# Performance work log

Hardware: AMD Instinct MI355X
Metric: run time of the kernel (lower is better)

The kernel has to match this reference:

```python
import jax, jax.numpy as jnp
import numpy as np
from jax import lax

B, CIN, IMG, K = 128, 3, 112, 7
C = 1024      # hidden_channels * channel_dilation
HID = 512     # hidden_channels
HW = (IMG // K) ** 2  # 256 patches
EPS = 1e-5


def _prelu(x, a):
    return jnp.where(x > 0, x, a * x)


def _bn(x, g, b):
    # BatchNorm2d with track_running_stats=False: always uses batch stats
    m = x.mean(axis=(0, 2, 3), keepdims=True)
    v = x.var(axis=(0, 2, 3), keepdims=True)
    return (x - m) * lax.rsqrt(v + EPS) * g[None, :, None, None] + b[None, :, None, None]


def setup_inputs() -> dict:
    key = jax.random.key(0)
    ks = jax.random.split(key, 16)
    d = {
        'x':  jax.random.normal(ks[0], (B, CIN, IMG, IMG), jnp.float32),
        'w0': jax.random.normal(ks[1], (C, CIN, K, K), jnp.float32) * 0.05,
        'b0': jax.random.normal(ks[2], (C,), jnp.float32) * 0.01,
        'a0': jnp.full((1,), 0.25, jnp.float32),
    }
    for i in range(1, 4):
        kw, kb = jax.random.split(jax.random.fold_in(key, i))
        d[f'w{i}'] = jax.random.normal(kw, (C, C), jnp.float32) * 0.02
        d[f'b{i}'] = jax.random.normal(kb, (C,), jnp.float32) * 0.01
        d[f'g{i}'] = jnp.ones((C,), jnp.float32)
        d[f'bt{i}'] = jnp.zeros((C,), jnp.float32)
        d[f'p{i}'] = jnp.full((1,), 0.25, jnp.float32)
    d['pos'] = jax.random.normal(ks[3], (1, HW, C), jnp.float32)
    d['am'] = jnp.full((1,), 0.25, jnp.float32)
    d['wm'] = jax.random.normal(ks[4], (HID, C), jnp.float32) * 0.03
    d['bm'] = jax.random.normal(ks[5], (HID,), jnp.float32) * 0.01
    pkeys = jax.random.split(ks[6], B)
    d['perm'] = jax.vmap(lambda k: jax.random.permutation(k, HW))(pkeys).astype(jnp.int32)
    return d


def reference(x, w0, b0, a0,
              w1, b1, g1, bt1, p1,
              w2, b2, g2, bt2, p2,
              w3, b3, g3, bt3, p3,
              pos, am, wm, bm, perm):
    # patch-embed conv: stride = kernel_size -> [B, C, 16, 16]
    h = lax.conv_general_dilated(x, w0, (K, K), 'VALID',
                                 dimension_numbers=('NCHW', 'OIHW', 'NCHW'))
    h = _prelu(h + b0[None, :, None, None], a0)
    for w, b, g, bt, p in ((w1, b1, g1, bt1, p1),
                           (w2, b2, g2, bt2, p2),
                           (w3, b3, g3, bt3, p3)):
        h = jnp.einsum('bchw,dc->bdhw', h, w) + b[None, :, None, None]  # 1x1 conv
        h = _prelu(_bn(h, g, bt), p)
    Bn, Cn, Hn, Wn = h.shape
    enc = h.reshape(Bn, Cn, Hn * Wn).transpose(0, 2, 1)  # [B, HW, C]
    enc = enc + pos                                      # private: add pos embedding
    enc = _prelu(enc, am) @ wm.T + bm                    # mixer -> [B, HW, HID]
    # private: per-sample token permutation (single batched gather)
    return jnp.take_along_axis(enc, perm[:, :, None], axis=1)
```

## Files before the change

kernel.cpp:

```cpp
#include <hip/hip_runtime.h>
#include <hip/hip_bf16.h>
#include <stdint.h>


typedef __attribute__((ext_vector_type(8))) short bf16x8;
typedef __attribute__((ext_vector_type(4))) float f32x4;

__device__ __forceinline__ float bf2f(uint32_t u) {
  union { uint32_t i; float f; } v; v.i = u << 16; return v.f;
}
__device__ __forceinline__ ushort f2bf(float f) {
  union { float f; uint32_t i; } v; v.f = f;
  uint32_t i = v.i;
  return (ushort)((i + 0x7FFFu + ((i >> 16) & 1u)) >> 16);
}

template<int EPI, int XB, int K, int DOUT>
__global__ void __launch_bounds__(512, 2)
gemm_kernel(const ushort* __restrict__ A, const ushort* __restrict__ Bw,
            const float* __restrict__ bias, const float* __restrict__ alpha,
            void* __restrict__ outp, float* __restrict__ part,
            const int* __restrict__ inv)
{
  __shared__ __align__(16) ushort At[2][256 * 64];
  __shared__ __align__(16) ushort Bt[3][256 * 64];
  const int tid  = threadIdx.x;
  const int lane = tid & 63;
  const int wid  = tid >> 6;
  const int wm   = wid >> 2;
  const int wn   = wid & 3;

  const int s = blockIdx.x;
  const int j = s >> 3;
  const int x = j & ((1 << XB) - 1);
  const int y = ((j >> XB) << 3) | (s & 7);
  const int t0 = y << 8;
  const int d0 = x << 8;

  f32x4 acc[8][4] = {};

  const int swz = (((lane >> 4) ^ (lane & 7)) << 4);
  const char* LA0 = (const char*)&At[0][0] + ((((wm << 7) + (lane & 15))) << 7) + swz;
  const char* LA1 = (const char*)&At[0][0] + ((((wm << 7) + (lane & 15))) << 7) + (swz ^ 64);
  const char* LB0 = (const char*)&Bt[0][0] + ((((wn << 6) + (lane & 15))) << 7) + swz;
  const char* LB1 = (const char*)&Bt[0][0] + ((((wn << 6) + (lane & 15))) << 7) + (swz ^ 64);

  const int lrow8 = lane >> 3;
  const int csrc  = (lane & 7) ^ lrow8;
  const ushort* gAw = A  + (size_t)(t0 + (wid << 4) + lrow8) * K + (csrc << 3);
  const ushort* gBw = Bw + (size_t)(d0 + (wid << 4) + lrow8) * K + (csrc << 3);
  char* stA = (char*)&At[0][0] + (wid << 11);
  char* stB = (char*)&Bt[0][0] + (wid << 11);

#define STAGE_A(T, BUF, H) do {                                                          \
    __builtin_amdgcn_global_load_lds(                                                    \
      (const __attribute__((address_space(1))) uint32_t*)(gAw + (size_t)((H)*128)*K + ((size_t)(T) << 6)),     \
      (__attribute__((address_space(3))) uint32_t*)(stA + (BUF)*32768 + (H)*16384), 16, 0, 0);                  \
    __builtin_amdgcn_global_load_lds(                                                    \
      (const __attribute__((address_space(1))) uint32_t*)(gAw + (size_t)((H)*128+8)*K + ((size_t)(T) << 6)),   \
      (__attribute__((address_space(3))) uint32_t*)(stA + (BUF)*32768 + (H)*16384 + 1024), 16, 0, 0);           \
  } while (0)
#define STAGE_B(T, BOFF, H) do {                                                         \
    __builtin_amdgcn_global_load_lds(                                                    \
      (const __attribute__((address_space(1))) uint32_t*)(gBw + (size_t)((H)*128)*K + ((size_t)(T) << 6)),     \
      (__attribute__((address_space(3))) uint32_t*)(stB + (BOFF) + (H)*16384), 16, 0, 0);                       \
    __builtin_amdgcn_global_load_lds(                                                    \
      (const __attribute__((address_space(1))) uint32_t*)(gBw + (size_t)((H)*128+8)*K + ((size_t)(T) << 6)),   \
      (__attribute__((address_space(3))) uint32_t*)(stB + (BOFF) + (H)*16384 + 1024), 16, 0, 0);                \
  } while (0)

#define RD_A(dst, BASE, CUR, MH) do {                                                    \
    dst[0] = *(const bf16x8*)((BASE) + (CUR)*32768 + (MH)*8192 + 0);                     \
    dst[1] = *(const bf16x8*)((BASE) + (CUR)*32768 + (MH)*8192 + 2048);                  \
    dst[2] = *(const bf16x8*)((BASE) + (CUR)*32768 + (MH)*8192 + 4096);                  \
    dst[3] = *(const bf16x8*)((BASE) + (CUR)*32768 + (MH)*8192 + 6144);                  \
  } while (0)
#define RD_B(dst, BASE, BOFF) do {                                                       \
    dst[0] = *(const bf16x8*)((BASE) + (BOFF) + 0);                                      \
    dst[1] = *(const bf16x8*)((BASE) + (BOFF) + 2048);                                   \
    dst[2] = *(const bf16x8*)((BASE) + (BOFF) + 4096);                                   \
    dst[3] = *(const bf16x8*)((BASE) + (BOFF) + 6144);                                   \
  } while (0)
#define MFMA16(AF, BF, MH) do {                                                          \
    __builtin_amdgcn_s_setprio(1);                                                       \
    _Pragma("unroll")                                                                    \
    for (int m_ = 0; m_ < 4; ++m_)                                                       \
      _Pragma("unroll")                                                                  \
      for (int n_ = 0; n_ < 4; ++n_)                                                     \
        acc[((MH) << 2) + m_][n_] = __builtin_amdgcn_mfma_f32_16x16x32_bf16(             \
            AF[m_], BF[n_], acc[((MH) << 2) + m_][n_], 0, 0, 0);                         \
    __builtin_amdgcn_s_setprio(0);                                                       \
  } while (0)

#define TILE_BODY(T, CUR, HN1, HN2) do {                                                 \
    if (HN1) { asm volatile("s_waitcnt vmcnt(4)" ::: "memory"); }                        \
    else     { asm volatile("s_waitcnt vmcnt(0)" ::: "memory"); }                        \
    __builtin_amdgcn_s_barrier();                                                        \
    RD_A(aX, LA0, CUR, 0);                                                               \
    RD_B(b0f, LB0, bR);                                                                  \
    if (HN1) { STAGE_A((T) + 1, (CUR) ^ 1, 0); STAGE_A((T) + 1, (CUR) ^ 1, 1); }         \
    if (HN2) { STAGE_B((T) + 2, bS, 0); STAGE_B((T) + 2, bS, 1); }                       \
    MFMA16(aX, b0f, 0);                                                                  \
    RD_A(aY, LA0, CUR, 1);                                                               \
    MFMA16(aY, b0f, 1);                                                                  \
    RD_A(aX, LA1, CUR, 0);                                                               \
    RD_B(b1f, LB1, bR);                                                                  \
    MFMA16(aX, b1f, 0);                                                                  \
    RD_A(aY, LA1, CUR, 1);                                                               \
    MFMA16(aY, b1f, 1);                                                                  \
    { int tmp_ = bR; bR = bN; bN = bS; bS = tmp_; }                                      \
  } while (0)

  constexpr int NT = K >> 6;

  STAGE_A(0, 0, 0); STAGE_A(0, 0, 1);
  STAGE_B(0, 0, 0); STAGE_B(0, 0, 1);
  STAGE_B(1, 32768, 0); STAGE_B(1, 32768, 1);

  int bR = 0, bN = 32768, bS = 65536;
  bf16x8 aX[4], aY[4], b0f[4], b1f[4];

  if constexpr ((NT & 1) == 0) {
#pragma unroll 1
    for (int tp = 0; tp < NT; tp += 2) {
      const bool m1 = (tp + 2 < NT);
      TILE_BODY(tp,     0, true, m1);
      TILE_BODY(tp + 1, 1, m1, m1);
    }
  } else {
#pragma unroll 1
    for (int t = 0; t < NT; ++t) {
      const int cur = t & 1;
      TILE_BODY(t, cur, (t + 1 < NT), (t + 2 < NT));
    }
  }

  float bs[4];
#pragma unroll
  for (int n = 0; n < 4; ++n) bs[n] = bias[d0 + (wn << 6) + (n << 4) + (lane & 15)];
  float a0v = (EPI == 0) ? alpha[0] : 0.0f;
  float sA[4] = {0.f, 0.f, 0.f, 0.f}, s2A[4] = {0.f, 0.f, 0.f, 0.f};

#pragma unroll
  for (int m = 0; m < 8; ++m) {
#pragma unroll
    for (int r = 0; r < 4; ++r) {
      int row = t0 + (wm << 7) + (m << 4) + ((lane >> 4) << 2) + r;
      int orow = (EPI == 2) ? ((row & ~255) | inv[row]) : row;
#pragma unroll
      for (int n = 0; n < 4; ++n) {
        int d = d0 + (wn << 6) + (n << 4) + (lane & 15);
        float v = acc[m][n][r] + bs[n];
        if (EPI == 0) v = v > 0.f ? v : a0v * v;
        if (EPI == 1) { sA[n] += v; s2A[n] += v * v; }
        if (EPI == 2) ((float*)outp)[(size_t)orow * DOUT + d] = v;
        else          ((ushort*)outp)[(size_t)row * DOUT + d] = f2bf(v);
      }
    }
  }

  if (EPI == 1) {
    float2* sm = (float2*)&At[0][0];
    int slot = (wm << 2) | (lane >> 4);
    __syncthreads();
#pragma unroll
    for (int n = 0; n < 4; ++n) {
      int c = (wn << 6) + (n << 4) + (lane & 15);
      sm[slot * 256 + c] = make_float2(sA[n], s2A[n]);
    }
    __syncthreads();
    if (tid < 256) {
      float ss = 0.f, ss2 = 0.f;
      for (int q = 0; q < 8; ++q) {
        float2 v = sm[q * 256 + tid];
        ss += v.x; ss2 += v.y;
      }
      part[(size_t)y * 2048 + d0 + tid]        = ss;
      part[(size_t)y * 2048 + 1024 + d0 + tid] = ss2;
    }
  }
#undef STAGE_A
#undef STAGE_B
#undef RD_A
#undef RD_B
#undef MFMA16
#undef TILE_BODY
}

__global__ void bnfold_kernel(const float* __restrict__ part, const float* __restrict__ g,
                              const float* __restrict__ bt, float* __restrict__ scsh) {
  int d = (blockIdx.x << 8) + threadIdx.x;
  float s = 0.f, s2 = 0.f;
  for (int j = 0; j < 128; ++j) { s += part[j * 2048 + d]; s2 += part[j * 2048 + 1024 + d]; }
  float mean = s * (1.f / 32768.f);
  float var  = s2 * (1.f / 32768.f) - mean * mean;
  float sc = g[d] * rsqrtf(var + 1e-5f);
  scsh[d] = sc;
  scsh[1024 + d] = bt[d] - mean * sc;
}

template<bool MIX>
__global__ void bnact_kernel(ushort* __restrict__ Y, const float* __restrict__ scsh,
                             const float* __restrict__ p, const float* __restrict__ pos,
                             const float* __restrict__ am) {
  float pp = p[0];
  float aa = MIX ? am[0] : 0.f;
#pragma unroll 1
  for (int it = 0; it < 8; ++it) {
    size_t vi = ((size_t)it << 19) + ((size_t)blockIdx.x << 8) + threadIdx.x;
    size_t i = vi << 3;
    int d = (int)(i & 1023);
    float pv[8];
    if (MIX) {
      int prow = (int)((i >> 10) & 255);
      const float4* pb = (const float4*)(pos + ((size_t)prow << 10) + d);
      float4 pA = pb[0], pB = pb[1];
      pv[0]=pA.x; pv[1]=pA.y; pv[2]=pA.z; pv[3]=pA.w;
      pv[4]=pB.x; pv[5]=pB.y; pv[6]=pB.z; pv[7]=pB.w;
    }
    uint4 raw = *(const uint4*)(Y + i);
    uint32_t w[4] = {raw.x, raw.y, raw.z, raw.w};
    uint32_t o[4];
#pragma unroll
    for (int q = 0; q < 4; ++q) {
      int dd = d + q * 2;
      float v0 = bf2f(w[q] & 0xFFFFu) * scsh[dd]     + scsh[1024 + dd];
      float v1 = bf2f(w[q] >> 16)     * scsh[dd + 1] + scsh[1024 + dd + 1];
      v0 = v0 > 0.f ? v0 : pp * v0;
      v1 = v1 > 0.f ? v1 : pp * v1;
      if (MIX) {
        v0 += pv[2 * q];     v1 += pv[2 * q + 1];
        v0 = v0 > 0.f ? v0 : aa * v0;
        v1 = v1 > 0.f ? v1 : aa * v1;
      }
      o[q] = (uint32_t)f2bf(v0) | ((uint32_t)f2bf(v1) << 16);
    }
    *(uint4*)(Y + i) = make_uint4(o[0], o[1], o[2], o[3]);
  }
}

__global__ void prep_kernel(const float* __restrict__ x,
                            const float* __restrict__ w0, const float* __restrict__ w1,
                            const float* __restrict__ w2, const float* __restrict__ w3,
                            const float* __restrict__ wm, const int* __restrict__ perm,
                            ushort* __restrict__ P, ushort* __restrict__ w0b,
                            ushort* __restrict__ w1b, ushort* __restrict__ w2b,
                            ushort* __restrict__ w3b, ushort* __restrict__ wmb,
                            int* __restrict__ inv) {
  const int b = blockIdx.x, tid = threadIdx.x;
  if (b < 2048) {
    if (tid < 192) {
      int t0 = b << 4;
#pragma unroll 1
      for (int tt = 0; tt < 16; ++tt) {
        int t = t0 + tt;
        ushort v = 0;
        if (tid < 147) {
          int bb = t >> 8, pidx = t & 255;
          int pi = pidx >> 4, pj = pidx & 15;
          int cin = tid / 49, rem = tid - cin * 49;
          int dy = rem / 7, dx = rem - dy * 7;
          v = f2bf(x[(size_t)(bb * 3 + cin) * 12544 + (size_t)(pi * 7 + dy) * 112 + (pj * 7 + dx)]);
        }
        P[(size_t)t * 192 + tid] = v;
      }
    }
  } else if (b < 4096) {
    int i = ((b - 2048) << 8) + tid;
#pragma unroll
    for (int r = 0; r < 2; ++r) {
      int idx = (r << 19) + i;
      w1b[idx] = f2bf(w1[idx]);
      w2b[idx] = f2bf(w2[idx]);
      w3b[idx] = f2bf(w3[idx]);
    }
    wmb[i] = f2bf(wm[i]);
  } else if (b < 4224) {
    int t = ((b - 4096) << 8) + tid;
    inv[(t & ~255) + perm[t]] = t & 255;
  } else {
    int d = b - 4224;
    if (tid < 192)
      w0b[d * 192 + tid] = (tid < 147) ? f2bf(w0[d * 147 + tid]) : (ushort)0;
  }
}

extern "C" void kernel_launch(void* const* d_in, const int* in_sizes, int n_in,
                              void* d_out, int out_size, void* d_ws, size_t ws_size,
                              hipStream_t stream) {
  const float* x   = (const float*)d_in[0];
  const float* w0  = (const float*)d_in[1];
  const float* b0  = (const float*)d_in[2];
  const float* a0  = (const float*)d_in[3];
  const float* w1  = (const float*)d_in[4];
  const float* b1  = (const float*)d_in[5];
  const float* g1  = (const float*)d_in[6];
  const float* bt1 = (const float*)d_in[7];
  const float* p1  = (const float*)d_in[8];
  const float* w2  = (const float*)d_in[9];
  const float* b2  = (const float*)d_in[10];
  const float* g2  = (const float*)d_in[11];
  const float* bt2 = (const float*)d_in[12];
  const float* p2  = (const float*)d_in[13];
  const float* w3  = (const float*)d_in[14];
  const float* b3  = (const float*)d_in[15];
  const float* g3  = (const float*)d_in[16];
  const float* bt3 = (const float*)d_in[17];
  const float* p3  = (const float*)d_in[18];
  const float* pos = (const float*)d_in[19];
  const float* am  = (const float*)d_in[20];
  const float* wm  = (const float*)d_in[21];
  const float* bm  = (const float*)d_in[22];
  const int*  perm = (const int*)d_in[23];

  char* ws = (char*)d_ws;
  ushort* B0   = (ushort*)ws;
  ushort* B1   = (ushort*)(ws + 67108864);
  float*  part = (float*)(ws + 134217728);
  float*  scsh = (float*)(ws + 134217728 + 2097152);
  int*    inv  = (int*)  (ws + 134217728 + 2097152 + 8192);
  char*   wb   = ws + 134217728 + 2097152 + 8192 + 131072;
  ushort* w1b  = (ushort*)wb;
  ushort* w2b  = w1b + 1048576;
  ushort* w3b  = w2b + 1048576;
  ushort* wmb  = w3b + 1048576;
  ushort* w0b  = wmb + 524288;

  prep_kernel<<<dim3(5248), dim3(256), 0, stream>>>(
      x, w0, w1, w2, w3, wm, perm, B1, w0b, w1b, w2b, w3b, wmb, inv);

  gemm_kernel<0, 2, 192, 1024><<<dim3(512), dim3(512), 0, stream>>>(
      B1, w0b, b0, a0, (void*)B0, nullptr, nullptr);

  gemm_kernel<1, 2, 1024, 1024><<<dim3(512), dim3(512), 0, stream>>>(
      B0, w1b, b1, nullptr, (void*)B1, part, nullptr);
  bnfold_kernel<<<dim3(4), dim3(256), 0, stream>>>(part, g1, bt1, scsh);
  bnact_kernel<false><<<dim3(2048), dim3(256), 0, stream>>>(B1, scsh, p1, nullptr, nullptr);

  gemm_kernel<1, 2, 1024, 1024><<<dim3(512), dim3(512), 0, stream>>>(
      B1, w2b, b2, nullptr, (void*)B0, part, nullptr);
  bnfold_kernel<<<dim3(4), dim3(256), 0, stream>>>(part, g2, bt2, scsh);
  bnact_kernel<false><<<dim3(2048), dim3(256), 0, stream>>>(B0, scsh, p2, nullptr, nullptr);

  gemm_kernel<1, 2, 1024, 1024><<<dim3(512), dim3(512), 0, stream>>>(
      B0, w3b, b3, nullptr, (void*)B1, part, nullptr);
  bnfold_kernel<<<dim3(4), dim3(256), 0, stream>>>(part, g3, bt3, scsh);
  bnact_kernel<true><<<dim3(2048), dim3(256), 0, stream>>>(B1, scsh, p3, pos, am);

  gemm_kernel<2, 1, 1024, 512><<<dim3(256), dim3(512), 0, stream>>>(
      B1, wmb, bm, nullptr, d_out, nullptr, inv);
}
```

Baseline: 385.4 us.

## Use 1024-thread GEMM blocks with 64x64 per-wave tiles

Doubles the GEMM block size from 8 to 16 waves while keeping the 256x256 block tile, so each wave computes a 64x64 sub-tile instead of 128x64. Global-to-LDS staging is split across more waves, with one load per wave per half instead of two, and the vmcnt waits and the BN partial-sum reduction are adjusted to match. The goal is more waves per CU to hide latency, at the cost of more LDS fragment reads per MFMA. It also relies on a launch bound of (1024,4), which could push the compiler into a very tight VGPR budget and cause spills.

```diff
diff --git a/kernel.cpp b/kernel.cpp
--- a/kernel.cpp
+++ b/kernel.cpp
@@ -16,7 +16,7 @@
 }
 
 template<int EPI, int XB, int K, int DOUT>
-__global__ void __launch_bounds__(512, 2)
+__global__ void __launch_bounds__(1024, 4)
 gemm_kernel(const ushort* __restrict__ A, const ushort* __restrict__ Bw,
             const float* __restrict__ bias, const float* __restrict__ alpha,
             void* __restrict__ outp, float* __restrict__ part,
@@ -37,77 +37,61 @@
   const int t0 = y << 8;
   const int d0 = x << 8;
 
-  f32x4 acc[8][4] = {};
+  f32x4 acc[4][4] = {};
 
   const int swz = (((lane >> 4) ^ (lane & 7)) << 4);
-  const char* LA0 = (const char*)&At[0][0] + ((((wm << 7) + (lane & 15))) << 7) + swz;
-  const char* LA1 = (const char*)&At[0][0] + ((((wm << 7) + (lane & 15))) << 7) + (swz ^ 64);
+  const char* LA0 = (const char*)&At[0][0] + ((((wm << 6) + (lane & 15))) << 7) + swz;
+  const char* LA1 = (const char*)&At[0][0] + ((((wm << 6) + (lane & 15))) << 7) + (swz ^ 64);
   const char* LB0 = (const char*)&Bt[0][0] + ((((wn << 6) + (lane & 15))) << 7) + swz;
   const char* LB1 = (const char*)&Bt[0][0] + ((((wn << 6) + (lane & 15))) << 7) + (swz ^ 64);
 
   const int lrow8 = lane >> 3;
   const int csrc  = (lane & 7) ^ lrow8;
-  const ushort* gAw = A  + (size_t)(t0 + (wid << 4) + lrow8) * K + (csrc << 3);
-  const ushort* gBw = Bw + (size_t)(d0 + (wid << 4) + lrow8) * K + (csrc << 3);
-  char* stA = (char*)&At[0][0] + (wid << 11);
-  char* stB = (char*)&Bt[0][0] + (wid << 11);
+  const ushort* gAw = A  + (size_t)(t0 + (wid << 3) + lrow8) * K + (csrc << 3);
+  const ushort* gBw = Bw + (size_t)(d0 + (wid << 3) + lrow8) * K + (csrc << 3);
+  char* stA = (char*)&At[0][0] + (wid << 10);
+  char* stB = (char*)&Bt[0][0] + (wid << 10);
 
 #define STAGE_A(T, BUF, H) do {                                                          \
     __builtin_amdgcn_global_load_lds(                                                    \
       (const __attribute__((address_space(1))) uint32_t*)(gAw + (size_t)((H)*128)*K + ((size_t)(T) << 6)),     \
       (__attribute__((address_space(3))) uint32_t*)(stA + (BUF)*32768 + (H)*16384), 16, 0, 0);                  \
-    __builtin_amdgcn_global_load_lds(                                                    \
-      (const __attribute__((address_space(1))) uint32_t*)(gAw + (size_t)((H)*128+8)*K + ((size_t)(T) << 6)),   \
-      (__attribute__((address_space(3))) uint32_t*)(stA + (BUF)*32768 + (H)*16384 + 1024), 16, 0, 0);           \
   } while (0)
 #define STAGE_B(T, BOFF, H) do {                                                         \
     __builtin_amdgcn_global_load_lds(                                                    \
       (const __attribute__((address_space(1))) uint32_t*)(gBw + (size_t)((H)*128)*K + ((size_t)(T) << 6)),     \
       (__attribute__((address_space(3))) uint32_t*)(stB + (BOFF) + (H)*16384), 16, 0, 0);                       \
-    __builtin_amdgcn_global_load_lds(                                                    \
-      (const __attribute__((address_space(1))) uint32_t*)(gBw + (size_t)((H)*128+8)*K + ((size_t)(T) << 6)),   \
-      (__attribute__((address_space(3))) uint32_t*)(stB + (BOFF) + (H)*16384 + 1024), 16, 0, 0);                \
-  } while (0)
-
-#define RD_A(dst, BASE, CUR, MH) do {                                                    \
-    dst[0] = *(const bf16x8*)((BASE) + (CUR)*32768 + (MH)*8192 + 0);                     \
-    dst[1] = *(const bf16x8*)((BASE) + (CUR)*32768 + (MH)*8192 + 2048);                  \
-    dst[2] = *(const bf16x8*)((BASE) + (CUR)*32768 + (MH)*8192 + 4096);                  \
-    dst[3] = *(const bf16x8*)((BASE) + (CUR)*32768 + (MH)*8192 + 6144);                  \
-  } while (0)
-#define RD_B(dst, BASE, BOFF) do {                                                       \
-    dst[0] = *(const bf16x8*)((BASE) + (BOFF) + 0);                                      \
-    dst[1] = *(const bf16x8*)((BASE) + (BOFF) + 2048);                                   \
-    dst[2] = *(const bf16x8*)((BASE) + (BOFF) + 4096);                                   \
-    dst[3] = *(const bf16x8*)((BASE) + (BOFF) + 6144);                                   \
-  } while (0)
-#define MFMA16(AF, BF, MH) do {                                                          \
+  } while (0)
+
+#define RD4(dst, BASE, OFF) do {                                                         \
+    dst[0] = *(const bf16x8*)((BASE) + (OFF) + 0);                                       \
+    dst[1] = *(const bf16x8*)((BASE) + (OFF) + 2048);                                    \
+    dst[2] = *(const bf16x8*)((BASE) + (OFF) + 4096);                                    \
+    dst[3] = *(const bf16x8*)((BASE) + (OFF) + 6144);                                    \
+  } while (0)
+#define MFMA44(AF, BF) do {                                                              \
     __builtin_amdgcn_s_setprio(1);                                                       \
     _Pragma("unroll")                                                                    \
     for (int m_ = 0; m_ < 4; ++m_)                                                       \
       _Pragma("unroll")                                                                  \
       for (int n_ = 0; n_ < 4; ++n_)                                                     \
-        acc[((MH) << 2) + m_][n_] = __builtin_amdgcn_mfma_f32_16x16x32_bf16(             \
-            AF[m_], BF[n_], acc[((MH) << 2) + m_][n_], 0, 0, 0);                         \
+        acc[m_][n_] = __builtin_amdgcn_mfma_f32_16x16x32_bf16(                           \
+            AF[m_], BF[n_], acc[m_][n_], 0, 0, 0);                                       \
     __builtin_amdgcn_s_setprio(0);                                                       \
   } while (0)
 
 #define TILE_BODY(T, CUR, HN1, HN2) do {                                                 \
-    if (HN1) { asm volatile("s_waitcnt vmcnt(4)" ::: "memory"); }                        \
+    if (HN1) { asm volatile("s_waitcnt vmcnt(2)" ::: "memory"); }                        \
     else     { asm volatile("s_waitcnt vmcnt(0)" ::: "memory"); }                        \
     __builtin_amdgcn_s_barrier();                                                        \
-    RD_A(aX, LA0, CUR, 0);                                                               \
-    RD_B(b0f, LB0, bR);                                                                  \
+    RD4(af, LA0, (CUR)*32768);                                                           \
+    RD4(bf_, LB0, bR);                                                                   \
     if (HN1) { STAGE_A((T) + 1, (CUR) ^ 1, 0); STAGE_A((T) + 1, (CUR) ^ 1, 1); }         \
     if (HN2) { STAGE_B((T) + 2, bS, 0); STAGE_B((T) + 2, bS, 1); }                       \
-    MFMA16(aX, b0f, 0);                                                                  \
-    RD_A(aY, LA0, CUR, 1);                                                               \
-    MFMA16(aY, b0f, 1);                                                                  \
-    RD_A(aX, LA1, CUR, 0);                                                               \
-    RD_B(b1f, LB1, bR);                                                                  \
-    MFMA16(aX, b1f, 0);                                                                  \
-    RD_A(aY, LA1, CUR, 1);                                                               \
-    MFMA16(aY, b1f, 1);                                                                  \
+    MFMA44(af, bf_);                                                                     \
+    RD4(af, LA1, (CUR)*32768);                                                           \
+    RD4(bf_, LB1, bR);                                                                   \
+    MFMA44(af, bf_);                                                                     \
     { int tmp_ = bR; bR = bN; bN = bS; bS = tmp_; }                                      \
   } while (0)
 
@@ -118,7 +102,7 @@
   STAGE_B(1, 32768, 0); STAGE_B(1, 32768, 1);
 
   int bR = 0, bN = 32768, bS = 65536;
-  bf16x8 aX[4], aY[4], b0f[4], b1f[4];
+  bf16x8 af[4], bf_[4];
 
   if constexpr ((NT & 1) == 0) {
 #pragma unroll 1
@@ -142,10 +126,10 @@
   float sA[4] = {0.f, 0.f, 0.f, 0.f}, s2A[4] = {0.f, 0.f, 0.f, 0.f};
 
 #pragma unroll
-  for (int m = 0; m < 8; ++m) {
+  for (int m = 0; m < 4; ++m) {
 #pragma unroll
     for (int r = 0; r < 4; ++r) {
-      int row = t0 + (wm << 7) + (m << 4) + ((lane >> 4) << 2) + r;
+      int row = t0 + (wm << 6) + (m << 4) + ((lane >> 4) << 2) + r;
       int orow = (EPI == 2) ? ((row & ~255) | inv[row]) : row;
 #pragma unroll
       for (int n = 0; n < 4; ++n) {
@@ -171,7 +155,7 @@
     __syncthreads();
     if (tid < 256) {
       float ss = 0.f, ss2 = 0.f;
-      for (int q = 0; q < 8; ++q) {
+      for (int q = 0; q < 16; ++q) {
         float2 v = sm[q * 256 + tid];
         ss += v.x; ss2 += v.y;
       }
@@ -181,9 +165,8 @@
   }
 #undef STAGE_A
 #undef STAGE_B
-#undef RD_A
-#undef RD_B
-#undef MFMA16
+#undef RD4
+#undef MFMA44
 #undef TILE_BODY
 }
 
@@ -329,24 +312,24 @@
   prep_kernel<<<dim3(5248), dim3(256), 0, stream>>>(
       x, w0, w1, w2, w3, wm, perm, B1, w0b, w1b, w2b, w3b, wmb, inv);
 
-  gemm_kernel<0, 2, 192, 1024><<<dim3(512), dim3(512), 0, stream>>>(
+  gemm_kernel<0, 2, 192, 1024><<<dim3(512), dim3(1024), 0, stream>>>(
       B1, w0b, b0, a0, (void*)B0, nullptr, nullptr);
 
-  gemm_kernel<1, 2, 1024, 1024><<<dim3(512), dim3(512), 0, stream>>>(
+  gemm_kernel<1, 2, 1024, 1024><<<dim3(512), dim3(1024), 0, stream>>>(
       B0, w1b, b1, nullptr, (void*)B1, part, nullptr);
   bnfold_kernel<<<dim3(4), dim3(256), 0, stream>>>(part, g1, bt1, scsh);
   bnact_kernel<false><<<dim3(2048), dim3(256), 0, stream>>>(B1, scsh, p1, nullptr, nullptr);
 
-  gemm_kernel<1, 2, 1024, 1024><<<dim3(512), dim3(512), 0, stream>>>(
+  gemm_kernel<1, 2, 1024, 1024><<<dim3(512), dim3(1024), 0, stream>>>(
       B1, w2b, b2, nullptr, (void*)B0, part, nullptr);
   bnfold_kernel<<<dim3(4), dim3(256), 0, stream>>>(part, g2, bt2, scsh);
   bnact_kernel<false><<<dim3(2048), dim3(256), 0, stream>>>(B0, scsh, p2, nullptr, nullptr);
 
-  gemm_kernel<1, 2, 1024, 1024><<<dim3(512), dim3(512), 0, stream>>>(
+  gemm_kernel<1, 2, 1024, 1024><<<dim3(512), dim3(1024), 0, stream>>>(
       B0, w3b, b3, nullptr, (void*)B1, part, nullptr);
   bnfold_kernel<<<dim3(4), dim3(256), 0, stream>>>(part, g3, bt3, scsh);
   bnact_kernel<true><<<dim3(2048), dim3(256), 0, stream>>>(B1, scsh, p3, pos, am);
 
-  gemm_kernel<2, 1, 1024, 512><<<dim3(256), dim3(512), 0, stream>>>(
+  gemm_kernel<2, 1, 1024, 512><<<dim3(256), dim3(1024), 0, stream>>>(
       B1, wmb, bm, nullptr, d_out, nullptr, inv);
 }
```

New measurement: 465.7 us. 1.21x slower.
